# Performance work log

Hardware: AMD Instinct MI355X
Metric: run time of the kernel (lower is better)

The kernel has to match this reference:

```python
import jax, jax.numpy as jnp
import numpy as np

D_MODEL, HQ, HKV = 2048, 32, 8
DK = D_MODEL // HQ          # 64
GROUP = HQ // HKV           # 4 query heads per kv head
B, S = 1, 2048


def setup_inputs() -> dict:
    key = jax.random.key(0)
    ks = jax.random.split(key, 5)
    sc = 0.02
    return {
        "x":  jax.random.normal(ks[0], (B, S, D_MODEL), jnp.float32),
        "wq": jax.random.normal(ks[1], (D_MODEL, D_MODEL), jnp.float32) * sc,
        "bq": jnp.zeros((D_MODEL,), jnp.float32),
        "wk": jax.random.normal(ks[2], (HKV * DK, D_MODEL), jnp.float32) * sc,
        "bk": jnp.zeros((HKV * DK,), jnp.float32),
        "wv": jax.random.normal(ks[3], (HKV * DK, D_MODEL), jnp.float32) * sc,
        "bv": jnp.zeros((HKV * DK,), jnp.float32),
        "wo": jax.random.normal(ks[4], (D_MODEL, D_MODEL), jnp.float32) * sc,
        "bo": jnp.zeros((D_MODEL,), jnp.float32),
    }


def reference(x, wq, bq, wk, bk, wv, bv, wo, bo):
    b, s, _ = x.shape
    scale = 1.0 / jnp.sqrt(jnp.asarray(DK, x.dtype))
    # projections (torch Linear: y = x @ W.T + b)
    q = (x @ wq.T + bq).reshape(b, s, HKV, GROUP, DK)   # [B,S,Hkv,G,Dk]
    k = (x @ wk.T + bk).reshape(b, s, HKV, DK)          # [B,S,Hkv,Dk]
    v = (x @ wv.T + bv).reshape(b, s, HKV, DK)
    # GQA: broadcast each kv head over its GROUP query heads (no repeat_interleave)
    scores = jnp.einsum("bshgd,bthd->bhgst", q, k) * scale   # [B,Hkv,G,S,S]
    causal = jnp.tril(jnp.ones((s, s), bool))
    scores = jnp.where(causal, scores, jnp.asarray(-jnp.inf, scores.dtype))
    attn = jax.nn.softmax(scores, axis=-1)
    out = jnp.einsum("bhgst,bthd->bshgd", attn, v)           # [B,S,Hkv,G,Dk]
    out = out.reshape(b, s, D_MODEL)
    return out @ wo.T + bo
```

## Files before the change

### kernel.cpp

```cpp
#include <hip/hip_runtime.h>


#define S_LEN 2048
#define DM    2048
#define QKVW  3072

typedef float  f32x4  __attribute__((ext_vector_type(4)));
typedef float  f32x16 __attribute__((ext_vector_type(16)));
typedef __bf16 bf16x8 __attribute__((ext_vector_type(8)));
typedef unsigned short u16;
typedef unsigned int   u32;
typedef u16 u16x8 __attribute__((ext_vector_type(8)));
typedef u16 u16x4 __attribute__((ext_vector_type(4)));
typedef u32 u32x4 __attribute__((ext_vector_type(4)));
typedef u32 u32x2 __attribute__((ext_vector_type(2)));

__device__ __forceinline__ u16 f2b(float f) {
    __bf16 h = (__bf16)f;
    return __builtin_bit_cast(unsigned short, h);
}
__device__ __forceinline__ u32 pk2(float lo, float hi) {
    return (u32)f2b(lo) | ((u32)f2b(hi) << 16);
}
__device__ __forceinline__ float max3f(float a, float b, float c) {
    return fmaxf(fmaxf(a, b), c);
}

__device__ __forceinline__ void xswap(u32 a, u32 b, u32& lo, u32& hi) {
#if __has_builtin(__builtin_amdgcn_permlane32_swap)
    u32x2 r = __builtin_amdgcn_permlane32_swap(a, b, false, false);
    lo = r[0]; hi = r[1];
#else
    const int hf = (threadIdx.x & 63) >> 5;
    const u32 sA = __shfl_xor(a, 32), sB = __shfl_xor(b, 32);
    lo = hf ? sB : a;
    hi = hf ? b : sA;
#endif
}
__device__ __forceinline__ float xhalf_max(float x) {
    u32 xb = __builtin_bit_cast(u32, x), lo, hi;
    xswap(xb, xb, lo, hi);
    return fmaxf(__builtin_bit_cast(float, lo), __builtin_bit_cast(float, hi));
}
__device__ __forceinline__ float xhalf_sum(float x) {
    u32 xb = __builtin_bit_cast(u32, x), lo, hi;
    xswap(xb, xb, lo, hi);
    return __builtin_bit_cast(float, lo) + __builtin_bit_cast(float, hi);
}

#define MFMA16(a, b, c) __builtin_amdgcn_mfma_f32_16x16x32_bf16((a), (b), (c), 0, 0, 0)
#define MFMA32(a, b, c) __builtin_amdgcn_mfma_f32_32x32x16_bf16((a), (b), (c), 0, 0, 0)

__device__ __forceinline__ void gld16(const void* g, void* l) {
    __builtin_amdgcn_global_load_lds(
        (const __attribute__((address_space(1))) void*)g,
        (__attribute__((address_space(3))) void*)l, 16, 0, 0);
}

__global__ __launch_bounds__(256) void cvt5(
    const float* __restrict__ x,  const float* __restrict__ wq,
    const float* __restrict__ wk, const float* __restrict__ wv,
    const float* __restrict__ bq, const float* __restrict__ bk,
    const float* __restrict__ bv,
    u16* __restrict__ xb, u16* __restrict__ wqkvb,
    float* __restrict__ bqkv)
{
    if (blockIdx.x == 5120) {
        for (int i = threadIdx.x; i < 3072; i += 256)
            bqkv[i] = (i < 2048) ? bq[i] : (i < 2560 ? bk[i - 2048] : bv[i - 2560]);
        return;
    }
    int i = blockIdx.x * 256 + threadIdx.x;
    const float* s; u16* d; int off;
    if      (i < 524288)  { s = x;  d = xb;    off = i; }
    else if (i < 1048576) { s = wq; d = wqkvb; off = i - 524288; }
    else if (i < 1179648) { s = wk; d = wqkvb + (size_t)2048 * 2048; off = i - 1048576; }
    else                  { s = wv; d = wqkvb + (size_t)2560 * 2048; off = i - 1179648; }
    const float4* s4 = (const float4*)s;
    float4 a = s4[2 * (size_t)off], b = s4[2 * (size_t)off + 1];
    u16x8 o;
    o[0] = f2b(a.x); o[1] = f2b(a.y); o[2] = f2b(a.z); o[3] = f2b(a.w);
    o[4] = f2b(b.x); o[5] = f2b(b.y); o[6] = f2b(b.z); o[7] = f2b(b.w);
    ((u16x8*)d)[(size_t)off] = o;
}

template <bool OUT_BF16, bool QSCALE, bool VFUSE>
__global__ __launch_bounds__(256) void gemm_nt64(
    const u16* __restrict__ A, const u16* __restrict__ B,
    const float* __restrict__ bias, void* __restrict__ Cv,
    u16* __restrict__ Vt,
    const float* __restrict__ wosrc, u16* __restrict__ wodst,
    int N, int K, int nxb, int ngemm)
{
    __shared__ u16 As[2][128 * 32];
    __shared__ u16 Bs[2][64 * 32];
    const int bid = blockIdx.x;

    if (VFUSE && bid >= ngemm) {
        const int i = (bid - ngemm) * 256 + threadIdx.x;
        const float4* s4 = (const float4*)wosrc;
        float4 a = s4[2 * (size_t)i], b = s4[2 * (size_t)i + 1];
        u16x8 o;
        o[0] = f2b(a.x); o[1] = f2b(a.y); o[2] = f2b(a.z); o[3] = f2b(a.w);
        o[4] = f2b(b.x); o[5] = f2b(b.y); o[6] = f2b(b.z); o[7] = f2b(b.w);
        ((u16x8*)wodst)[(size_t)i] = o;
        return;
    }

    const int wg  = (bid & 7) * (ngemm >> 3) + (bid >> 3);
    const int bm  = (wg / nxb) * 128;
    const int bn  = (wg % nxb) * 64;

    const int tid  = threadIdx.x;
    const int lane = tid & 63;
    const int w    = tid >> 6;
    const int wr   = w >> 1, wc = w & 1;
    const int la = lane & 15, lg = lane >> 4;

    f32x4 acc[4][2] = {};

    char* const abase = (char*)&As[0][0] + w * 1024;
    char* const bbase = (char*)&Bs[0][0] + w * 1024;

    for (int k0 = 0; k0 < K; k0 += 64) {
        #pragma unroll
        for (int i = 0; i < 4; ++i) {
            const int c   = tid + 256 * i;
            const int kh  = c >> 9;
            const int rem = c & 511;
            const int row = rem >> 2;
            const int seg = rem & 3;
            gld16(A + (size_t)(bm + row) * K + k0 + kh * 32 + seg * 8,
                  abase + i * 4096);
        }
        #pragma unroll
        for (int i = 0; i < 2; ++i) {
            const int c   = tid + 256 * i;
            const int kh  = c >> 8;
            const int rem = c & 255;
            const int row = rem >> 2;
            const int seg = rem & 3;
            gld16(B + (size_t)(bn + row) * K + k0 + kh * 32 + seg * 8,
                  bbase + i * 4096);
        }
        __syncthreads();
        #pragma unroll
        for (int kh = 0; kh < 2; ++kh) {
            bf16x8 af[4], bf[2];
            #pragma unroll
            for (int m = 0; m < 4; ++m)
                af[m] = *(const bf16x8*)(&As[kh][0] + (wr * 64 + m * 16 + la) * 32 + lg * 8);
            #pragma unroll
            for (int n = 0; n < 2; ++n)
                bf[n] = *(const bf16x8*)(&Bs[kh][0] + (wc * 32 + n * 16 + la) * 32 + lg * 8);
            #pragma unroll
            for (int m = 0; m < 4; ++m)
                #pragma unroll
                for (int n = 0; n < 2; ++n)
                    acc[m][n] = MFMA16(af[m], bf[n], acc[m][n]);
        }
        __syncthreads();
    }

    if (VFUSE && bn >= 2560) {
        #pragma unroll
        for (int m = 0; m < 4; ++m) {
            #pragma unroll
            for (int n = 0; n < 2; ++n) {
                const int col = bn + wc * 32 + n * 16 + la;
                const float bb = bias[col];
                u16x4 pk;
                #pragma unroll
                for (int j = 0; j < 4; ++j)
                    pk[j] = f2b(acc[m][n][j] + bb);
                const int row0 = bm + wr * 64 + m * 16 + lg * 4;
                *(u16x4*)&Vt[(size_t)(col - 2560) * S_LEN + row0] = pk;
            }
        }
        return;
    }

    #pragma unroll
    for (int m = 0; m < 4; ++m) {
        #pragma unroll
        for (int n = 0; n < 2; ++n) {
            const int col = bn + wc * 32 + n * 16 + la;
            const float bb = bias[col];
            const float osc = (QSCALE && col < 2048) ? 0.180336881f : 1.0f;
            #pragma unroll
            for (int j = 0; j < 4; ++j) {
                const int row = bm + wr * 64 + m * 16 + lg * 4 + j;
                const float v = (acc[m][n][j] + bb) * osc;
                if (OUT_BF16) ((u16*)Cv)[(size_t)row * N + col] = f2b(v);
                else          ((float*)Cv)[(size_t)row * N + col] = v;
            }
        }
    }
}

__global__ __launch_bounds__(512, 4) void attn(
    const u16* __restrict__ QKVb,
    const u16* __restrict__ Vt,
    u16* __restrict__ Ob)
{
    const int tid  = threadIdx.x;
    const int lane = tid & 63;
    const int w    = tid >> 6;
    const int head = w & 3;
    const int par  = w >> 2;
    const int bid  = blockIdx.x;
    const int band = (bid < 256) ? (63 - (bid >> 3)) : ((bid - 256) >> 3);
    const int h    = bid & 7;
    const int hq   = h * 4 + head;
    const int q0   = band * 32;
    const int lq   = lane & 31;
    const int hi   = lane >> 5;

    __shared__ char LDS[65536];

    bf16x8 qf[4];
    #pragma unroll
    for (int ds = 0; ds < 4; ++ds)
        qf[ds] = *(const bf16x8*)&QKVb[(size_t)(q0 + lq) * QKVW + hq * 64 + ds * 16 + hi * 8];

    f32x16 ot[2] = {};
    float m = -3e38f, lsum = 0.f;

    const char* Khb = (const char*)QKVb + 4096 + h * 128;
    const char* Vhb = (const char*)(Vt + (size_t)h * 64 * S_LEN);

    const int r0 = tid >> 3;
    const int s0 = (((tid & 7) ^ (r0 & 7)) << 4);
    const int woff = w * 1024;

    const int nch = (band >> 1) + 1;
    const int nit = (nch + 1) >> 1;

    auto stage_pair = [&](int j) {
        const int pb = (j & 1) * 16384;
        const size_t kr = (size_t)(j * 128 + r0);
        gld16(Khb + kr * 6144 + s0,          LDS + pb + woff);
        gld16(Khb + (kr + 64) * 6144 + s0,   LDS + pb + 8192 + woff);
        const size_t vb = ((size_t)r0 << 12) + (size_t)(j * 256) + s0;
        gld16(Vhb + vb,        LDS + 32768 + pb + woff);
        gld16(Vhb + vb + 128,  LDS + 32768 + pb + 8192 + woff);
    };

    stage_pair(0);
    __syncthreads();

    for (int i = 0; i < nit; ++i) {
        if (i + 1 < nit) stage_pair(i + 1);

        const int cg = 2 * i + par;
        if (cg < nch) {
            const int base = (i & 1) * 16384 + par * 8192;
            const char* Kb = LDS + base;
            const char* Vb = LDS + 32768 + base;
            const int k0 = cg * 64;

            f32x16 s[2];
            __builtin_amdgcn_s_setprio(1);
            #pragma unroll
            for (int kt = 0; kt < 2; ++kt) {
                f32x16 acc = {};
                #pragma unroll
                for (int ds = 0; ds < 4; ++ds) {
                    const int key = kt * 32 + lq;
                    const int byteK = (key << 7) + ((ds * 32 + hi * 16) ^ ((key & 7) << 4));
                    bf16x8 kf = *(const bf16x8*)(Kb + byteK);
                    acc = MFMA32(kf, qf[ds], acc);
                }
                s[kt] = acc;
            }
            __builtin_amdgcn_s_setprio(0);

            if (k0 + 63 > q0) {
                #pragma unroll
                for (int kt = 0; kt < 2; ++kt)
                    #pragma unroll
                    for (int r = 0; r < 16; ++r) {
                        const int key = k0 + kt * 32 + (r & 3) + 8 * (r >> 2) + 4 * hi;
                        if (key > q0 + lq) s[kt][r] = -1e30f;
                    }
            }

            float t10[11];
            #pragma unroll
            for (int r = 0; r < 10; ++r)
                t10[r] = max3f(s[(3*r) >> 4][(3*r) & 15],
                               s[(3*r+1) >> 4][(3*r+1) & 15],
                               s[(3*r+2) >> 4][(3*r+2) & 15]);
            t10[10] = fmaxf(s[1][14], s[1][15]);
            const float x0 = max3f(t10[0], t10[1], t10[2]);
            const float x1 = max3f(t10[3], t10[4], t10[5]);
            const float x2 = max3f(t10[6], t10[7], t10[8]);
            const float x3 = fmaxf(t10[9], t10[10]);
            const float pm = xhalf_max(fmaxf(max3f(x0, x1, x2), x3));

            if (!__all(pm <= m + 11.5f)) {
                const float mn   = fmaxf(m, pm);
                const float corr = __builtin_exp2f(m - mn);
                m = mn;
                lsum *= corr;
                #pragma unroll
                for (int r = 0; r < 16; ++r) {
                    const int row = (r & 3) + 8 * (r >> 2) + 4 * hi;
                    const float cr = __shfl(corr, row);
                    ot[0][r] *= cr;
                    ot[1][r] *= cr;
                }
            }

            #pragma unroll
            for (int kt = 0; kt < 2; ++kt)
                #pragma unroll
                for (int r = 0; r < 16; ++r)
                    s[kt][r] = __builtin_exp2f(s[kt][r] - m);
            float tsum[16];
            #pragma unroll
            for (int r = 0; r < 16; ++r) tsum[r] = s[0][r] + s[1][r];
            #pragma unroll
            for (int st = 8; st >= 1; st >>= 1)
                #pragma unroll
                for (int r = 0; r < 8; ++r)
                    if (r < st) tsum[r] += tsum[r + st];
            lsum += xhalf_sum(tsum[0]);

            bf16x8 pa[4];
            #pragma unroll
            for (int kb = 0; kb < 4; ++kb) {
                const int kt = kb >> 1;
                const int rb = (kb & 1) * 8;
                const u32 A = pk2(s[kt][rb + 0], s[kt][rb + 1]);
                const u32 B = pk2(s[kt][rb + 4], s[kt][rb + 5]);
                const u32 C = pk2(s[kt][rb + 2], s[kt][rb + 3]);
                const u32 D = pk2(s[kt][rb + 6], s[kt][rb + 7]);
                u32 e0, e1, e2, e3;
                xswap(A, B, e0, e2);
                xswap(C, D, e1, e3);
                u32x4 t4;
                t4[0] = e0; t4[1] = e1; t4[2] = e2; t4[3] = e3;
                pa[kb] = __builtin_bit_cast(bf16x8, t4);
            }

            __builtin_amdgcn_s_setprio(1);
            #pragma unroll
            for (int dt = 0; dt < 2; ++dt)
                #pragma unroll
                for (int kb = 0; kb < 4; ++kb) {
                    const int d = dt * 32 + lq;
                    const int byteV = (d << 7) + ((kb * 32 + hi * 16) ^ ((d & 7) << 4));
                    bf16x8 vf = *(const bf16x8*)(Vb + byteV);
                    ot[dt] = MFMA32(pa[kb], vf, ot[dt]);
                }
            __builtin_amdgcn_s_setprio(0);
        }

        __syncthreads();
    }

    float* Uls = (float*)LDS;
    float* Mls = (float*)(LDS + 32768);
    float* Lls = (float*)(LDS + 33280);

    if (par == 1) {
        #pragma unroll
        for (int r = 0; r < 16; ++r) {
            const int row = (r & 3) + 8 * (r >> 2) + 4 * hi;
            Uls[(head * 32 + row) * 64 + lq]      = ot[0][r];
            Uls[(head * 32 + row) * 64 + 32 + lq] = ot[1][r];
        }
        if (lane < 32) { Mls[head * 32 + lane] = m; Lls[head * 32 + lane] = lsum; }
    }
    __syncthreads();
    if (par == 1) return;

    const float m1  = Mls[head * 32 + lq];
    const float l1  = Lls[head * 32 + lq];
    const float M   = fmaxf(m, m1);
    const float a0  = __builtin_exp2f(m - M);
    const float a1  = __builtin_exp2f(m1 - M);
    const float inv = 1.f / (a0 * lsum + a1 * l1);

    #pragma unroll
    for (int r = 0; r < 16; ++r) {
        const int row = (r & 3) + 8 * (r >> 2) + 4 * hi;
        const float a0r = __shfl(a0, row);
        const float a1r = __shfl(a1, row);
        const float ivr = __shfl(inv, row);
        #pragma unroll
        for (int dt = 0; dt < 2; ++dt) {
            const float u1 = Uls[(head * 32 + row) * 64 + dt * 32 + lq];
            Ob[(size_t)(q0 + row) * DM + hq * 64 + dt * 32 + lq] =
                f2b((a0r * ot[dt][r] + a1r * u1) * ivr);
        }
    }
}

extern "C" void kernel_launch(void* const* d_in, const int* in_sizes, int n_in,
                              void* d_out, int out_size, void* d_ws, size_t ws_size,
                              hipStream_t stream)
{
    const float* x  = (const float*)d_in[0];
    const float* wq = (const float*)d_in[1];
    const float* bq = (const float*)d_in[2];
    const float* wk = (const float*)d_in[3];
    const float* bk = (const float*)d_in[4];
    const float* wv = (const float*)d_in[5];
    const float* bv = (const float*)d_in[6];
    const float* wo = (const float*)d_in[7];
    const float* bo = (const float*)d_in[8];
    float* out = (float*)d_out;

    char* ws = (char*)d_ws;
    u16* xb     = (u16*)(ws);
    u16* wqkvb  = (u16*)(ws + (8u  << 20));
    u16* wob    = (u16*)(ws + (20u << 20));
    u16* QKVb   = (u16*)(ws + (28u << 20));
    float* bqkv = (float*)(ws + (40u << 20));
    u16* Ob = xb;
    u16* Vt = (u16*)(ws + (41u << 20));

    cvt5<<<5121, 256, 0, stream>>>(x, wq, wk, wv, bq, bk, bv, xb, wqkvb, bqkv);
    gemm_nt64<true, true, true><<<768 + 2048, 256, 0, stream>>>(
        xb, wqkvb, bqkv, QKVb, Vt, wo, wob, QKVW, 2048, QKVW / 64, 768);
    attn<<<512, 512, 0, stream>>>(QKVb, Vt, Ob);
    gemm_nt64<false, false, false><<<512, 256, 0, stream>>>(
        Ob, wob, bo, out, nullptr, nullptr, nullptr, DM, 2048, DM / 64, 512);
}
```

Baseline: 127.9 us.

## Split attention KV loop across four wave groups with 1024-thread blocks

The attention kernel now launches 1024 threads per block, so four wave groups per head each handle one 32-key slice of every 128-key window, where before two groups each handled a 64-key chunk. Each window's K and V are staged in one double-buffered load, and the four partial softmax states are merged by a two-level tree reduction through LDS. The aim is more parallelism and latency hiding per block on short causal bands. The cost is more block-wide syncs, more merge work, fewer MFMAs per wave per barrier, and less room for concurrent blocks per CU.

```diff
diff --git a/kernel.cpp b/kernel.cpp
--- a/kernel.cpp
+++ b/kernel.cpp
@@ -198,7 +198,7 @@
     }
 }
 
-__global__ __launch_bounds__(512, 4) void attn(
+__global__ __launch_bounds__(1024, 8) void attn(
     const u16* __restrict__ QKVb,
     const u16* __restrict__ Vt,
     u16* __restrict__ Ob)
@@ -216,7 +216,9 @@
     const int lq   = lane & 31;
     const int hi   = lane >> 5;
 
-    __shared__ char LDS[65536];
+    __shared__ char  LDS[65536];
+    __shared__ float Ms[2][4][32];
+    __shared__ float Ls[2][4][32];
 
     bf16x8 qf[4];
     #pragma unroll
@@ -229,74 +231,61 @@
     const char* Khb = (const char*)QKVb + 4096 + h * 128;
     const char* Vhb = (const char*)(Vt + (size_t)h * 64 * S_LEN);
 
-    const int r0 = tid >> 3;
-    const int s0 = (((tid & 7) ^ (r0 & 7)) << 4);
+    const int nkeys = q0 + 32;
+    const int nwin  = (nkeys + 127) >> 7;
+
+    const int krow = tid >> 3;
+    const int kslb = (((tid & 7) ^ (krow & 7)) << 4);
+    const int vd   = tid >> 4;
+    const int vslb = (((tid & 15) ^ (vd & 7)) << 4);
     const int woff = w * 1024;
 
-    const int nch = (band >> 1) + 1;
-    const int nit = (nch + 1) >> 1;
-
-    auto stage_pair = [&](int j) {
-        const int pb = (j & 1) * 16384;
-        const size_t kr = (size_t)(j * 128 + r0);
-        gld16(Khb + kr * 6144 + s0,          LDS + pb + woff);
-        gld16(Khb + (kr + 64) * 6144 + s0,   LDS + pb + 8192 + woff);
-        const size_t vb = ((size_t)r0 << 12) + (size_t)(j * 256) + s0;
-        gld16(Vhb + vb,        LDS + 32768 + pb + woff);
-        gld16(Vhb + vb + 128,  LDS + 32768 + pb + 8192 + woff);
+    auto stage_win = [&](int j) {
+        char* const base = LDS + (j & 1) * 32768;
+        gld16(Khb + (size_t)(j * 128 + krow) * 6144 + kslb, base + woff);
+        gld16(Vhb + ((size_t)vd << 12) + (size_t)j * 256 + vslb, base + 16384 + woff);
     };
 
-    stage_pair(0);
+    stage_win(0);
     __syncthreads();
 
-    for (int i = 0; i < nit; ++i) {
-        if (i + 1 < nit) stage_pair(i + 1);
-
-        const int cg = 2 * i + par;
-        if (cg < nch) {
-            const int base = (i & 1) * 16384 + par * 8192;
-            const char* Kb = LDS + base;
-            const char* Vb = LDS + 32768 + base;
-            const int k0 = cg * 64;
-
-            f32x16 s[2];
-            __builtin_amdgcn_s_setprio(1);
-            #pragma unroll
-            for (int kt = 0; kt < 2; ++kt) {
+    for (int i = 0; i < nwin; ++i) {
+        if (i + 1 < nwin) stage_win(i + 1);
+
+        const int k0w = i * 128 + par * 32;
+        if (k0w < nkeys) {
+            const char* Kb = LDS + (i & 1) * 32768;
+            const char* Vb = Kb + 16384;
+
+            f32x16 s;
+            {
                 f32x16 acc = {};
+                __builtin_amdgcn_s_setprio(1);
                 #pragma unroll
                 for (int ds = 0; ds < 4; ++ds) {
-                    const int key = kt * 32 + lq;
+                    const int key = par * 32 + lq;
                     const int byteK = (key << 7) + ((ds * 32 + hi * 16) ^ ((key & 7) << 4));
                     bf16x8 kf = *(const bf16x8*)(Kb + byteK);
                     acc = MFMA32(kf, qf[ds], acc);
                 }
-                s[kt] = acc;
-            }
-            __builtin_amdgcn_s_setprio(0);
-
-            if (k0 + 63 > q0) {
-                #pragma unroll
-                for (int kt = 0; kt < 2; ++kt)
-                    #pragma unroll
-                    for (int r = 0; r < 16; ++r) {
-                        const int key = k0 + kt * 32 + (r & 3) + 8 * (r >> 2) + 4 * hi;
-                        if (key > q0 + lq) s[kt][r] = -1e30f;
-                    }
-            }
-
-            float t10[11];
-            #pragma unroll
-            for (int r = 0; r < 10; ++r)
-                t10[r] = max3f(s[(3*r) >> 4][(3*r) & 15],
-                               s[(3*r+1) >> 4][(3*r+1) & 15],
-                               s[(3*r+2) >> 4][(3*r+2) & 15]);
-            t10[10] = fmaxf(s[1][14], s[1][15]);
-            const float x0 = max3f(t10[0], t10[1], t10[2]);
-            const float x1 = max3f(t10[3], t10[4], t10[5]);
-            const float x2 = max3f(t10[6], t10[7], t10[8]);
-            const float x3 = fmaxf(t10[9], t10[10]);
-            const float pm = xhalf_max(fmaxf(max3f(x0, x1, x2), x3));
+                __builtin_amdgcn_s_setprio(0);
+                s = acc;
+            }
+
+            if (k0w + 31 > q0) {
+                #pragma unroll
+                for (int r = 0; r < 16; ++r) {
+                    const int key = k0w + (r & 3) + 8 * (r >> 2) + 4 * hi;
+                    if (key > q0 + lq) s[r] = -1e30f;
+                }
+            }
+
+            float a8[8];
+            #pragma unroll
+            for (int r = 0; r < 8; ++r) a8[r] = fmaxf(s[r], s[r + 8]);
+            const float pm = xhalf_max(max3f(max3f(a8[0], a8[1], a8[2]),
+                                             max3f(a8[3], a8[4], a8[5]),
+                                             fmaxf(a8[6], a8[7])));
 
             if (!__all(pm <= m + 11.5f)) {
                 const float mn   = fmaxf(m, pm);
@@ -313,29 +302,25 @@
             }
 
             #pragma unroll
-            for (int kt = 0; kt < 2; ++kt)
-                #pragma unroll
-                for (int r = 0; r < 16; ++r)
-                    s[kt][r] = __builtin_exp2f(s[kt][r] - m);
-            float tsum[16];
-            #pragma unroll
-            for (int r = 0; r < 16; ++r) tsum[r] = s[0][r] + s[1][r];
-            #pragma unroll
-            for (int st = 8; st >= 1; st >>= 1)
-                #pragma unroll
-                for (int r = 0; r < 8; ++r)
-                    if (r < st) tsum[r] += tsum[r + st];
-            lsum += xhalf_sum(tsum[0]);
-
-            bf16x8 pa[4];
-            #pragma unroll
-            for (int kb = 0; kb < 4; ++kb) {
-                const int kt = kb >> 1;
-                const int rb = (kb & 1) * 8;
-                const u32 A = pk2(s[kt][rb + 0], s[kt][rb + 1]);
-                const u32 B = pk2(s[kt][rb + 4], s[kt][rb + 5]);
-                const u32 C = pk2(s[kt][rb + 2], s[kt][rb + 3]);
-                const u32 D = pk2(s[kt][rb + 6], s[kt][rb + 7]);
+            for (int r = 0; r < 16; ++r) s[r] = __builtin_exp2f(s[r] - m);
+            float t8[8];
+            #pragma unroll
+            for (int r = 0; r < 8; ++r) t8[r] = s[r] + s[r + 8];
+            #pragma unroll
+            for (int st = 4; st >= 1; st >>= 1)
+                #pragma unroll
+                for (int r = 0; r < 4; ++r)
+                    if (r < st) t8[r] += t8[r + st];
+            lsum += xhalf_sum(t8[0]);
+
+            bf16x8 pa[2];
+            #pragma unroll
+            for (int kb = 0; kb < 2; ++kb) {
+                const int rb = kb * 8;
+                const u32 A = pk2(s[rb + 0], s[rb + 1]);
+                const u32 B = pk2(s[rb + 4], s[rb + 5]);
+                const u32 C = pk2(s[rb + 2], s[rb + 3]);
+                const u32 D = pk2(s[rb + 6], s[rb + 7]);
                 u32 e0, e1, e2, e3;
                 xswap(A, B, e0, e2);
                 xswap(C, D, e1, e3);
@@ -348,9 +333,10 @@
             #pragma unroll
             for (int dt = 0; dt < 2; ++dt)
                 #pragma unroll
-                for (int kb = 0; kb < 4; ++kb) {
+                for (int kb = 0; kb < 2; ++kb) {
                     const int d = dt * 32 + lq;
-                    const int byteV = (d << 7) + ((kb * 32 + hi * 16) ^ ((d & 7) << 4));
+                    const int byteV = (d << 8) +
+                        ((par * 64 + kb * 32 + hi * 16) ^ ((d & 7) << 4));
                     bf16x8 vf = *(const bf16x8*)(Vb + byteV);
                     ot[dt] = MFMA32(pa[kb], vf, ot[dt]);
                 }
@@ -360,40 +346,72 @@
         __syncthreads();
     }
 
-    float* Uls = (float*)LDS;
-    float* Mls = (float*)(LDS + 32768);
-    float* Lls = (float*)(LDS + 33280);
-
-    if (par == 1) {
+    if (par >= 2) {
+        float* U = (float*)(LDS + (par - 2) * 32768);
         #pragma unroll
         for (int r = 0; r < 16; ++r) {
             const int row = (r & 3) + 8 * (r >> 2) + 4 * hi;
-            Uls[(head * 32 + row) * 64 + lq]      = ot[0][r];
-            Uls[(head * 32 + row) * 64 + 32 + lq] = ot[1][r];
-        }
-        if (lane < 32) { Mls[head * 32 + lane] = m; Lls[head * 32 + lane] = lsum; }
+            U[(head * 32 + row) * 64 + lq]      = ot[0][r];
+            U[(head * 32 + row) * 64 + 32 + lq] = ot[1][r];
+        }
+        if (lane < 32) { Ms[par - 2][head][lane] = m; Ls[par - 2][head][lane] = lsum; }
     }
     __syncthreads();
-    if (par == 1) return;
-
-    const float m1  = Mls[head * 32 + lq];
-    const float l1  = Lls[head * 32 + lq];
-    const float M   = fmaxf(m, m1);
-    const float a0  = __builtin_exp2f(m - M);
-    const float a1  = __builtin_exp2f(m1 - M);
-    const float inv = 1.f / (a0 * lsum + a1 * l1);
-
-    #pragma unroll
-    for (int r = 0; r < 16; ++r) {
-        const int row = (r & 3) + 8 * (r >> 2) + 4 * hi;
-        const float a0r = __shfl(a0, row);
-        const float a1r = __shfl(a1, row);
-        const float ivr = __shfl(inv, row);
-        #pragma unroll
-        for (int dt = 0; dt < 2; ++dt) {
-            const float u1 = Uls[(head * 32 + row) * 64 + dt * 32 + lq];
-            Ob[(size_t)(q0 + row) * DM + hq * 64 + dt * 32 + lq] =
-                f2b((a0r * ot[dt][r] + a1r * u1) * ivr);
+    if (par < 2) {
+        float* U = (float*)(LDS + par * 32768);
+        const float m1 = Ms[par][head][lq];
+        const float l1 = Ls[par][head][lq];
+        const float M  = fmaxf(m, m1);
+        const float a0 = __builtin_exp2f(m - M);
+        const float a1 = __builtin_exp2f(m1 - M);
+        m = M;
+        lsum = a0 * lsum + a1 * l1;
+        #pragma unroll
+        for (int r = 0; r < 16; ++r) {
+            const int row = (r & 3) + 8 * (r >> 2) + 4 * hi;
+            const float a0r = __shfl(a0, row);
+            const float a1r = __shfl(a1, row);
+            #pragma unroll
+            for (int dt = 0; dt < 2; ++dt) {
+                const float u1 = U[(head * 32 + row) * 64 + dt * 32 + lq];
+                ot[dt][r] = a0r * ot[dt][r] + a1r * u1;
+            }
+        }
+    }
+    __syncthreads();
+    if (par == 1) {
+        float* U = (float*)LDS;
+        #pragma unroll
+        for (int r = 0; r < 16; ++r) {
+            const int row = (r & 3) + 8 * (r >> 2) + 4 * hi;
+            U[(head * 32 + row) * 64 + lq]      = ot[0][r];
+            U[(head * 32 + row) * 64 + 32 + lq] = ot[1][r];
+        }
+        if (lane < 32) { Ms[0][head][lane] = m; Ls[0][head][lane] = lsum; }
+    }
+    __syncthreads();
+    if (par != 0) return;
+
+    {
+        float* U = (float*)LDS;
+        const float m1  = Ms[0][head][lq];
+        const float l1  = Ls[0][head][lq];
+        const float M   = fmaxf(m, m1);
+        const float a0  = __builtin_exp2f(m - M);
+        const float a1  = __builtin_exp2f(m1 - M);
+        const float inv = 1.f / (a0 * lsum + a1 * l1);
+        #pragma unroll
+        for (int r = 0; r < 16; ++r) {
+            const int row = (r & 3) + 8 * (r >> 2) + 4 * hi;
+            const float a0r = __shfl(a0, row);
+            const float a1r = __shfl(a1, row);
+            const float ivr = __shfl(inv, row);
+            #pragma unroll
+            for (int dt = 0; dt < 2; ++dt) {
+                const float u1 = U[(head * 32 + row) * 64 + dt * 32 + lq];
+                Ob[(size_t)(q0 + row) * DM + hq * 64 + dt * 32 + lq] =
+                    f2b((a0r * ot[dt][r] + a1r * u1) * ivr);
+            }
         }
     }
 }
@@ -425,7 +443,7 @@
     cvt5<<<5121, 256, 0, stream>>>(x, wq, wk, wv, bq, bk, bv, xb, wqkvb, bqkv);
     gemm_nt64<true, true, true><<<768 + 2048, 256, 0, stream>>>(
         xb, wqkvb, bqkv, QKVb, Vt, wo, wob, QKVW, 2048, QKVW / 64, 768);
-    attn<<<512, 512, 0, stream>>>(QKVb, Vt, Ob);
+    attn<<<512, 1024, 0, stream>>>(QKVb, Vt, Ob);
     gemm_nt64<false, false, false><<<512, 256, 0, stream>>>(
         Ob, wob, bo, out, nullptr, nullptr, nullptr, DM, 2048, DM / 64, 512);
 }
```

After: 399.9 us. 3.13x slower.
